# Optimization experiments

Hardware: AMD Instinct MI355X
Metric: run time of the kernel (lower is better)

The kernel has to match this reference:

```python
import jax, jax.numpy as jnp
import numpy as np

N, E, G = 50000, 800000, 64
NODE_DIM, HID, HEADS, EDGE_DIM = 128, 256, 4, 2
LAYER_IN = [NODE_DIM, HID, HID]
LAYER_HEADS = [HEADS, HEADS, 1]
BN_EPS = 1e-5


def setup_inputs() -> dict:
    key = jax.random.key(0)
    ks = iter(jax.random.split(key, 80))
    def nrm(shape, s=0.05):
        return jax.random.normal(next(ks), shape, jnp.float32) * s
    inp = {}
    inp['x'] = jax.random.normal(next(ks), (N, NODE_DIM), jnp.float32)
    inp['edge_index'] = jax.random.randint(next(ks), (2, E), 0, N, jnp.int32)
    inp['edge_attr'] = jax.random.normal(next(ks), (E, EDGE_DIM), jnp.float32)
    inp['batch'] = jnp.sort(jax.random.randint(next(ks), (N,), 0, G, jnp.int32))
    for i in range(3):
        H = LAYER_HEADS[i]; C = HID // H
        inp[f'W{i}'] = nrm((LAYER_IN[i], H * C))
        inp[f'asrc{i}'] = nrm((H, C))
        inp[f'adst{i}'] = nrm((H, C))
        inp[f'We{i}'] = nrm((EDGE_DIM, H * C))
        inp[f'aedge{i}'] = nrm((H, C))
        inp[f'bconv{i}'] = jnp.zeros((HID,), jnp.float32)
        inp[f'bn{i}_g'] = jnp.ones((HID,), jnp.float32)
        inp[f'bn{i}_b'] = jnp.zeros((HID,), jnp.float32)
        inp[f'bn{i}_m'] = nrm((HID,), 0.01)
        inp[f'bn{i}_v'] = jnp.ones((HID,), jnp.float32)
    inp['Wskip'] = nrm((NODE_DIM, HID))
    inp['bskip'] = jnp.zeros((HID,), jnp.float32)
    inp['Wp1'] = nrm((2 * HID, HID))
    inp['bp1'] = jnp.zeros((HID,), jnp.float32)
    inp['Wp2'] = nrm((HID, 1))
    inp['bp2'] = jnp.zeros((1,), jnp.float32)
    return inp


def gat_conv(x, src, dst, ea, W, a_s, a_d, We, a_e, b, H, concat):
    n = x.shape[0]
    C = W.shape[1] // H
    h = (x @ W).reshape(n, H, C)                      # [N,H,C]
    # attention logits per edge (src/dst node terms + edge term)
    al = ((h * a_s).sum(-1)[src]
          + (h * a_d).sum(-1)[dst]
          + ((ea @ We).reshape(-1, H, C) * a_e).sum(-1))  # [Et,H]
    al = jax.nn.leaky_relu(al, 0.2)
    # segment softmax over destination nodes
    amax = jax.ops.segment_max(al, dst, num_segments=n)
    ex = jnp.exp(al - amax[dst])
    den = jax.ops.segment_sum(ex, dst, num_segments=n)
    alpha = ex / (den[dst] + 1e-16)
    out = jax.ops.segment_sum(h[src] * alpha[..., None], dst, num_segments=n)  # [N,H,C]
    out = out.reshape(n, H * C) if concat else out.mean(axis=1)
    return out + b


def _forward(x, edge_index, edge_attr, batch, layer_params, Wskip, bskip, Wp1, bp1, Wp2, bp2):
    n = x.shape[0]
    # add self-loops (PyG GATConv default), edge_attr filled with mean
    loop = jnp.arange(n, dtype=edge_index.dtype)
    src = jnp.concatenate([edge_index[0], loop])
    dst = jnp.concatenate([edge_index[1], loop])
    ea = jnp.concatenate([edge_attr, jnp.broadcast_to(edge_attr.mean(0), (n, edge_attr.shape[1]))], axis=0)
    identity = x
    for i, (W, a_s, a_d, We, a_e, b, g, be, rm, rv) in enumerate(layer_params):
        layer_identity = (identity @ Wskip + bskip) if i == 0 else identity
        concat = i < 2
        H = LAYER_HEADS[i]
        h = gat_conv(x, src, dst, ea, W, a_s, a_d, We, a_e, b, H, concat)
        h = (h - rm) * jax.lax.rsqrt(rv + BN_EPS) * g + be   # BatchNorm1d (eval)
        h = jax.nn.elu(h)
        x = h + layer_identity
        identity = x
    # global mean + max pool per graph
    counts = jnp.maximum(jax.ops.segment_sum(jnp.ones((n,), x.dtype), batch, num_segments=G), 1.0)
    mean_pool = jax.ops.segment_sum(x, batch, num_segments=G) / counts[:, None]
    max_pool = jax.ops.segment_max(x, batch, num_segments=G)
    emb = jnp.concatenate([mean_pool, max_pool], axis=1)      # [G, 2*HID]
    hmid = jax.nn.relu(emb @ Wp1 + bp1)
    return hmid @ Wp2 + bp2                                   # [G, 1]


def reference(x, edge_index, edge_attr, batch,
              W0, asrc0, adst0, We0, aedge0, bconv0, bn0_g, bn0_b, bn0_m, bn0_v,
              W1, asrc1, adst1, We1, aedge1, bconv1, bn1_g, bn1_b, bn1_m, bn1_v,
              W2, asrc2, adst2, We2, aedge2, bconv2, bn2_g, bn2_b, bn2_m, bn2_v,
              Wskip, bskip, Wp1, bp1, Wp2, bp2):
    layer_params = [
        (W0, asrc0, adst0, We0, aedge0, bconv0, bn0_g, bn0_b, bn0_m, bn0_v),
        (W1, asrc1, adst1, We1, aedge1, bconv1, bn1_g, bn1_b, bn1_m, bn1_v),
        (W2, asrc2, adst2, We2, aedge2, bconv2, bn2_g, bn2_b, bn2_m, bn2_v),
    ]
    return _forward(x, edge_index, edge_attr, batch, layer_params, Wskip, bskip, Wp1, bp1, Wp2, bp2)
```

## Files before the change

### kernel.cpp

```cpp
#include <hip/hip_runtime.h>
#include <cfloat>

#define Nn 50000
#define Ee 800000
#define Etot (Ee + Nn)
#define Gg 64
#define HIDc 256
#define BN_EPS 1e-5f

typedef unsigned int   uint32;
typedef unsigned short ushort16;
typedef short  bf16x8 __attribute__((ext_vector_type(8)));
typedef float  f32x4  __attribute__((ext_vector_type(4)));

__device__ inline ushort16 f2bf(float f) {
    uint32 u = __float_as_uint(f);
    u = (u + 0x7fffu + ((u >> 16) & 1u)) >> 16;
    return (ushort16)u;
}
__device__ inline uint32 pack2(float a, float b) {
    return (uint32)f2bf(a) | ((uint32)f2bf(b) << 16);
}
__device__ inline uint32 fenc(float f) {
    uint32 b = __float_as_uint(f);
    return (b & 0x80000000u) ? ~b : (b | 0x80000000u);
}
__device__ inline float fdec(uint32 u) {
    uint32 b = (u & 0x80000000u) ? (u & 0x7fffffffu) : ~u;
    return __uint_as_float(b);
}

__device__ inline long ws_index(int c, int k, int KB) {
    int cb = c >> 4, m = c & 15, kb = k >> 5, q = (k >> 3) & 3, e = k & 7;
    return (((long)(cb * KB + kb) * 64 + q * 16 + m) << 3) + e;
}

#define CVT4 (Nn * 128 / 4)
#define CVT_BLKS ((CVT4 + 255) / 256)
#define EBKS ((Etot + 255) / 256)
__global__ __launch_bounds__(256) void prep_kernel(
        const float* __restrict__ ea, float* __restrict__ ea_s,
        const float* __restrict__ We0, const float* __restrict__ ae0,
        const float* __restrict__ We1, const float* __restrict__ ae1,
        const float* __restrict__ We2, const float* __restrict__ ae2,
        float* __restrict__ M,
        const float* __restrict__ W0, const float* __restrict__ Wskip,
        const float* __restrict__ W1, const float* __restrict__ W2,
        ushort16* __restrict__ WtC, ushort16* __restrict__ Wt1,
        ushort16* __restrict__ Wt2,
        const float* __restrict__ x, ushort16* __restrict__ xbf,
        const int* __restrict__ ei, int* __restrict__ counts) {
    int bid = blockIdx.x, t = threadIdx.x;
    if (bid < 256) {
        __shared__ float sh0[256], sh1[256];
        float s0 = 0.f, s1 = 0.f;
        for (int e = bid * 256 + t; e < Ee; e += 256 * 256) {
            s0 += ea[2 * e];
            s1 += ea[2 * e + 1];
        }
        sh0[t] = s0; sh1[t] = s1;
        __syncthreads();
        for (int off = 128; off > 0; off >>= 1) {
            if (t < off) { sh0[t] += sh0[t + off]; sh1[t] += sh1[t + off]; }
            __syncthreads();
        }
        if (t == 0) { atomicAdd(&ea_s[0], sh0[0]); atomicAdd(&ea_s[1], sh1[0]); }
    } else if (bid == 256) {
        if (t >= 18) return;
        int l = t < 8 ? 0 : (t < 16 ? 1 : 2);
        int r = t - l * 8;
        const float* We = (l == 0) ? We0 : (l == 1 ? We1 : We2);
        const float* ae = (l == 0) ? ae0 : (l == 1 ? ae1 : ae2);
        int Hl = (l < 2) ? 4 : 1;
        int Cl = 256 / Hl;
        int d = r / Hl, hh = r % Hl;
        float s = 0.f;
        for (int c = 0; c < Cl; ++c)
            s += We[d * 256 + hh * Cl + c] * ae[hh * Cl + c];
        M[l * 8 + r] = s;
    } else if (bid < 385) {
        int k = bid - 257;
        WtC[ws_index(t, k, 4)] = f2bf(W0[(long)k * 256 + t]);
    } else if (bid < 513) {
        int k = bid - 385;
        WtC[ws_index(256 + t, k, 4)] = f2bf(Wskip[(long)k * 256 + t]);
    } else if (bid < 769) {
        int k = bid - 513;
        Wt1[ws_index(t, k, 8)] = f2bf(W1[(long)k * 256 + t]);
    } else if (bid < 1025) {
        int k = bid - 769;
        Wt2[ws_index(t, k, 8)] = f2bf(W2[(long)k * 256 + t]);
    } else if (bid < 1025 + CVT_BLKS) {
        int i = (bid - 1025) * 256 + t;
        if (i < CVT4) {
            float4 v = *(const float4*)&x[i * 4];
            ushort4 o;
            o.x = f2bf(v.x); o.y = f2bf(v.y); o.z = f2bf(v.z); o.w = f2bf(v.w);
            *(ushort4*)&xbf[i * 4] = o;
        }
    } else {
        int e = (bid - 1025 - CVT_BLKS) * 256 + t;
        if (e < Etot) {
            int d = (e < Ee) ? ei[Ee + e] : (e - Ee);
            atomicAdd(&counts[d], 1);
        }
    }
}

__global__ void scan1_kernel(const int* __restrict__ in, int* __restrict__ inc,
                             int* __restrict__ bsums) {
    __shared__ int sh[256];
    int i = blockIdx.x * 256 + threadIdx.x;
    int v = (i < Nn) ? in[i] : 0;
    sh[threadIdx.x] = v;
    __syncthreads();
    for (int off = 1; off < 256; off <<= 1) {
        int t = ((int)threadIdx.x >= off) ? sh[threadIdx.x - off] : 0;
        __syncthreads();
        sh[threadIdx.x] += t;
        __syncthreads();
    }
    if (i < Nn) inc[i] = sh[threadIdx.x];
    if (threadIdx.x == 255) bsums[blockIdx.x] = sh[255];
}

__global__ void scan23_kernel(const int* __restrict__ inc, const int* __restrict__ bsums,
                              int* __restrict__ row_start, int* __restrict__ cursor, int nb) {
    __shared__ int sh[256];
    int b = blockIdx.x, t = threadIdx.x;
    sh[t] = (t < b && t < nb) ? bsums[t] : 0;
    __syncthreads();
    for (int off = 128; off > 0; off >>= 1) {
        if (t < off) sh[t] += sh[t + off];
        __syncthreads();
    }
    int base = sh[0];
    int i = b * 256 + t;
    if (i < Nn) {
        int v = inc[i] + base;
        row_start[i + 1] = v;
        cursor[i + 1] = v;
    }
    if (i == 0) { row_start[0] = 0; cursor[0] = 0; }
}

__global__ void scatter_kernel(const int* __restrict__ ei, const float* __restrict__ ea,
                               const float* __restrict__ ea_sum, int* __restrict__ cursor,
                               int* __restrict__ src_sorted, float* __restrict__ ea_sorted) {
    int e = blockIdx.x * blockDim.x + threadIdx.x;
    if (e >= Etot) return;
    int s, d; float e0, e1;
    if (e < Ee) {
        s = ei[e]; d = ei[Ee + e];
        e0 = ea[2 * e]; e1 = ea[2 * e + 1];
    } else {
        s = d = e - Ee;
        const float invE = 1.f / (float)Ee;
        e0 = ea_sum[0] * invE; e1 = ea_sum[1] * invE;
    }
    int pos = atomicAdd(&cursor[d], 1);
    src_sorted[pos] = s;
    ea_sorted[2 * pos]     = e0;
    ea_sorted[2 * pos + 1] = e1;
}

#define LDK 40
__global__ __launch_bounds__(256) void mfma_gemm_kernel(
        const ushort16* __restrict__ A,
        const ushort16* __restrict__ WS,
        uint32* __restrict__ outF,
        uint32* __restrict__ outS,
        const float* __restrict__ bskip,
        const float* __restrict__ a_s, const float* __restrict__ a_d,
        float* __restrict__ ssrc, float* __restrict__ sdst,
        int n, int K) {
    __shared__ ushort16 As[128 * LDK];
    const int t    = threadIdx.x;
    const int row0 = blockIdx.x * 128;
    const int c0   = blockIdx.y * 128;
    const bool isSkip = (outS != nullptr) && (c0 >= 256);
    const int cc0  = isSkip ? c0 - 256 : c0;
    const int wave = t >> 6, lane = t & 63;
    const int wr = wave >> 1, wc = wave & 1;
    const int l15 = lane & 15, quad = lane >> 4;
    const int KB = K >> 5;

    f32x4 acc[4][4];
#pragma unroll
    for (int j = 0; j < 4; ++j)
#pragma unroll
        for (int i = 0; i < 4; ++i) {
            acc[j][i][0] = 0.f; acc[j][i][1] = 0.f;
            acc[j][i][2] = 0.f; acc[j][i][3] = 0.f;
        }

    const int sm = t & 127;
    const int so = t >> 7;

    for (int k0 = 0; k0 < K; k0 += 32) {
        const int kb = k0 >> 5;
#pragma unroll
        for (int h = 0; h < 2; ++h) {
            int oct = so + 2 * h;
            int grow = row0 + sm;
            uint4 va = make_uint4(0, 0, 0, 0);
            if (grow < n) va = *(const uint4*)&A[(long)grow * K + k0 + 8 * oct];
            *(uint4*)&As[sm * LDK + 8 * oct] = va;
        }
        bf16x8 bfv[4];
#pragma unroll
        for (int j = 0; j < 4; ++j) {
            int cb = ((c0 + wc * 64) >> 4) + j;
            bfv[j] = *(const bf16x8*)&WS[(((long)cb * KB + kb) * 64 + lane) << 3];
        }
        __syncthreads();
        bf16x8 af[4];
#pragma unroll
        for (int i = 0; i < 4; ++i)
            af[i] = *(const bf16x8*)&As[(wr * 64 + i * 16 + l15) * LDK + quad * 8];
#pragma unroll
        for (int j = 0; j < 4; ++j)
#pragma unroll
            for (int i = 0; i < 4; ++i)
                acc[j][i] = __builtin_amdgcn_mfma_f32_16x16x32_bf16(
                    bfv[j], af[i], acc[j][i], 0, 0, 0);
        __syncthreads();
    }

    float4 bb[4];
#pragma unroll
    for (int j = 0; j < 4; ++j) {
        if (isSkip) bb[j] = *(const float4*)&bskip[cc0 + wc * 64 + j * 16 + quad * 4];
        else        bb[j] = make_float4(0.f, 0.f, 0.f, 0.f);
    }

    uint32* tgt = isSkip ? outS : outF;
#pragma unroll
    for (int i = 0; i < 4; ++i) {
        int row = row0 + wr * 64 + i * 16 + l15;
        if (row >= n) continue;
#pragma unroll
        for (int j = 0; j < 4; ++j) {
            int col = cc0 + wc * 64 + j * 16 + quad * 4;
            uint2 pk;
            pk.x = pack2(acc[j][i][0] + bb[j].x, acc[j][i][1] + bb[j].y);
            pk.y = pack2(acc[j][i][2] + bb[j].z, acc[j][i][3] + bb[j].w);
            *(uint2*)&tgt[(long)row * 128 + (col >> 1)] = pk;
        }
    }

    if (!isSkip && a_s != nullptr) {
        float4 asv[4], adv[4];
#pragma unroll
        for (int j = 0; j < 4; ++j) {
            int col = cc0 + wc * 64 + j * 16 + quad * 4;
            asv[j] = *(const float4*)&a_s[col];
            adv[j] = *(const float4*)&a_d[col];
        }
        const int part = (cc0 + wc * 64) >> 6;
#pragma unroll
        for (int i = 0; i < 4; ++i) {
            float ps = 0.f, pd = 0.f;
#pragma unroll
            for (int j = 0; j < 4; ++j) {
                ps += acc[j][i][0] * asv[j].x + acc[j][i][1] * asv[j].y
                    + acc[j][i][2] * asv[j].z + acc[j][i][3] * asv[j].w;
                pd += acc[j][i][0] * adv[j].x + acc[j][i][1] * adv[j].y
                    + acc[j][i][2] * adv[j].z + acc[j][i][3] * adv[j].w;
            }
            ps += __shfl_xor(ps, 16); ps += __shfl_xor(ps, 32);
            pd += __shfl_xor(pd, 16); pd += __shfl_xor(pd, 32);
            if (quad == 0) {
                int row = row0 + wr * 64 + i * 16 + l15;
                if (row < n) {
                    ssrc[row * 4 + part] = ps;
                    sdst[row * 4 + part] = pd;
                }
            }
        }
    }
}

template <int H>
__global__ __launch_bounds__(128) void agg_kernel(
        const int* __restrict__ src_sorted, const int* __restrict__ row_start,
        const float* __restrict__ ea_sorted, const float* __restrict__ ssrc,
        const float* __restrict__ sdst, const float* __restrict__ M,
        float* __restrict__ wbig,
        const uint32* __restrict__ hbuf2, const float* __restrict__ bconv,
        const float* __restrict__ bn_g, const float* __restrict__ bn_b,
        const float* __restrict__ bn_m, const float* __restrict__ bn_v,
        const uint32* __restrict__ identity2, uint32* __restrict__ out2) {
    __shared__ float shw[256 * H];
    int node = blockIdx.x;
    int t = threadIdx.x;
    int beg = row_start[node], end = row_start[node + 1];
    int deg = end - beg;
    bool big = deg > 256;

    if (t < 64) {
        int lane = t;
        float sd[H], M0[H], M1[H], m[H], den[H];
        if (H == 4) {
#pragma unroll
            for (int h = 0; h < H; ++h) sd[h] = sdst[node * 4 + h];
        } else {
            float4 v = *(const float4*)&sdst[node * 4];
            sd[0] = v.x + v.y + v.z + v.w;
        }
#pragma unroll
        for (int h = 0; h < H; ++h) {
            M0[h] = M[h]; M1[h] = M[H + h];
            m[h] = -FLT_MAX; den[h] = 0.f;
        }
        auto ssval = [&](int s, int h) -> float {
            if (H == 4) return ssrc[s * 4 + h];
            float4 v = *(const float4*)&ssrc[s * 4];
            return v.x + v.y + v.z + v.w;
        };
        if (!big) {
            float lreg[4][H];
#pragma unroll
            for (int k = 0; k < 4; ++k) {
                int idx = beg + lane + (k << 6);
                if (idx < end) {
                    int s = src_sorted[idx];
                    float e0 = ea_sorted[2 * idx], e1 = ea_sorted[2 * idx + 1];
#pragma unroll
                    for (int h = 0; h < H; ++h) {
                        float l = ssval(s, h) + sd[h] + e0 * M0[h] + e1 * M1[h];
                        l = (l > 0.f) ? l : 0.2f * l;
                        lreg[k][h] = l;
                        if (l > m[h]) { den[h] = den[h] * __expf(m[h] - l) + 1.f; m[h] = l; }
                        else den[h] += __expf(l - m[h]);
                    }
                }
            }
#pragma unroll
            for (int h = 0; h < H; ++h) {
                for (int off = 32; off > 0; off >>= 1) {
                    float om = __shfl_down(m[h], off);
                    float od = __shfl_down(den[h], off);
                    float nm = fmaxf(m[h], om);
                    den[h] = den[h] * __expf(m[h] - nm) + od * __expf(om - nm);
                    m[h] = nm;
                }
                m[h]   = __shfl(m[h], 0);
                den[h] = __shfl(den[h], 0);
                den[h] = 1.f / (den[h] + 1e-16f);
            }
#pragma unroll
            for (int k = 0; k < 4; ++k) {
                int idx = beg + lane + (k << 6);
                if (idx < end) {
#pragma unroll
                    for (int h = 0; h < H; ++h)
                        shw[(idx - beg) * H + h] = __expf(lreg[k][h] - m[h]) * den[h];
                }
            }
        } else {
            for (int idx = beg + lane; idx < end; idx += 64) {
                int s = src_sorted[idx];
                float e0 = ea_sorted[2 * idx], e1 = ea_sorted[2 * idx + 1];
#pragma unroll
                for (int h = 0; h < H; ++h) {
                    float l = ssval(s, h) + sd[h] + e0 * M0[h] + e1 * M1[h];
                    l = (l > 0.f) ? l : 0.2f * l;
                    wbig[(long)idx * H + h] = l;
                    if (l > m[h]) { den[h] = den[h] * __expf(m[h] - l) + 1.f; m[h] = l; }
                    else den[h] += __expf(l - m[h]);
                }
            }
#pragma unroll
            for (int h = 0; h < H; ++h) {
                for (int off = 32; off > 0; off >>= 1) {
                    float om = __shfl_down(m[h], off);
                    float od = __shfl_down(den[h], off);
                    float nm = fmaxf(m[h], om);
                    den[h] = den[h] * __expf(m[h] - nm) + od * __expf(om - nm);
                    m[h] = nm;
                }
                m[h]   = __shfl(m[h], 0);
                den[h] = __shfl(den[h], 0);
                den[h] = 1.f / (den[h] + 1e-16f);
            }
            for (int idx = beg + lane; idx < end; idx += 64) {
#pragma unroll
                for (int h = 0; h < H; ++h) {
                    float l = wbig[(long)idx * H + h];
                    wbig[(long)idx * H + h] = __expf(l - m[h]) * den[h];
                }
            }
        }
    }
    __syncthreads();

    int c2 = t;
    const int C2 = 128 / H;
    int hh = c2 / C2;
    float a0 = 0.f, a1 = 0.f;
    for (int idx = beg; idx < end; idx += 4) {
        int   s[4];
        float ww[4];
#pragma unroll
        for (int k = 0; k < 4; ++k) {
            int j = idx + k;
            bool ok = j < end;
            int jj = ok ? j : beg;
            s[k]  = src_sorted[jj];
            float wv = big ? wbig[(long)jj * H + hh] : shw[(jj - beg) * H + hh];
            ww[k] = ok ? wv : 0.f;
        }
#pragma unroll
        for (int k = 0; k < 4; ++k) {
            uint32 u = hbuf2[(long)s[k] * 128 + c2];
            float lo = __uint_as_float(u << 16);
            float hi = __uint_as_float(u & 0xffff0000u);
            a0 += ww[k] * lo;
            a1 += ww[k] * hi;
        }
    }
    int c = 2 * c2;
    float v0 = a0 + bconv[c];
    float v1 = a1 + bconv[c + 1];
    v0 = (v0 - bn_m[c])     * rsqrtf(bn_v[c]     + BN_EPS) * bn_g[c]     + bn_b[c];
    v1 = (v1 - bn_m[c + 1]) * rsqrtf(bn_v[c + 1] + BN_EPS) * bn_g[c + 1] + bn_b[c + 1];
    v0 = (v0 > 0.f) ? v0 : (expf(v0) - 1.f);
    v1 = (v1 > 0.f) ? v1 : (expf(v1) - 1.f);
    uint32 idu = identity2[(long)node * 128 + c2];
    v0 += __uint_as_float(idu << 16);
    v1 += __uint_as_float(idu & 0xffff0000u);
    out2[(long)node * 128 + c2] = pack2(v0, v1);
}

#define POOL_ROWS 32
__global__ __launch_bounds__(128) void pool_kernel(
        const uint32* __restrict__ x2, const int* __restrict__ batch,
        float* __restrict__ psum, uint32* __restrict__ pmax, float* __restrict__ pcnt) {
    int c2 = threadIdx.x;
    int n0 = blockIdx.x * POOL_ROWS;
    if (n0 >= Nn) return;
    int n1 = min(n0 + POOL_ROWS, Nn);
    int cur = batch[n0];
    float s0 = 0.f, s1 = 0.f, m0 = -FLT_MAX, m1 = -FLT_MAX;
    int cnt = 0;
    int c = 2 * c2;
    for (int i = n0; i < n1; ++i) {
        int g = batch[i];
        if (g != cur) {
            atomicAdd(&psum[cur * 256 + c], s0);
            atomicAdd(&psum[cur * 256 + c + 1], s1);
            atomicMax(&pmax[cur * 256 + c], fenc(m0));
            atomicMax(&pmax[cur * 256 + c + 1], fenc(m1));
            if (c2 == 0) atomicAdd(&pcnt[cur], (float)cnt);
            cur = g; s0 = s1 = 0.f; m0 = m1 = -FLT_MAX; cnt = 0;
        }
        uint32 u = x2[(long)i * 128 + c2];
        float lo = __uint_as_float(u << 16);
        float hi = __uint_as_float(u & 0xffff0000u);
        s0 += lo; s1 += hi;
        m0 = fmaxf(m0, lo); m1 = fmaxf(m1, hi);
        ++cnt;
    }
    atomicAdd(&psum[cur * 256 + c], s0);
    atomicAdd(&psum[cur * 256 + c + 1], s1);
    atomicMax(&pmax[cur * 256 + c], fenc(m0));
    atomicMax(&pmax[cur * 256 + c + 1], fenc(m1));
    if (c2 == 0) atomicAdd(&pcnt[cur], (float)cnt);
}

__global__ __launch_bounds__(256) void mlp_kernel(
        const float* __restrict__ psum, const uint32* __restrict__ pmax,
        const float* __restrict__ pcnt, const float* __restrict__ Wp1,
        const float* __restrict__ bp1, const float* __restrict__ Wp2,
        const float* __restrict__ bp2, float* __restrict__ out) {
    int g = blockIdx.x;
    int j = threadIdx.x;
    float inv = 1.f / fmaxf(pcnt[g], 1.f);
    float acc = bp1[j];
    for (int k = 0; k < 256; ++k)
        acc += (psum[g * 256 + k] * inv) * Wp1[k * 256 + j];
    for (int k = 0; k < 256; ++k)
        acc += fdec(pmax[g * 256 + k]) * Wp1[(256 + k) * 256 + j];
    float v = fmaxf(acc, 0.f) * Wp2[j];
    __shared__ float red[256];
    red[j] = v;
    __syncthreads();
    for (int off = 128; off > 0; off >>= 1) {
        if (j < off) red[j] += red[j + off];
        __syncthreads();
    }
    if (j == 0) out[g] = red[0] + bp2[0];
}

extern "C" void kernel_launch(void* const* d_in, const int* in_sizes, int n_in,
                              void* d_out, int out_size, void* d_ws, size_t ws_size,
                              hipStream_t stream) {
    const float* x   = (const float*)d_in[0];
    const int*   ei  = (const int*)d_in[1];
    const float* ea  = (const float*)d_in[2];
    const int*   bat = (const int*)d_in[3];
    auto LP = [&](int l, int j) { return (const float*)d_in[4 + l * 10 + j]; };
    const float* Wskip = (const float*)d_in[34];
    const float* bskip = (const float*)d_in[35];
    const float* Wp1   = (const float*)d_in[36];
    const float* bp1   = (const float*)d_in[37];
    const float* Wp2   = (const float*)d_in[38];
    const float* bp2   = (const float*)d_in[39];
    float* out = (float*)d_out;

    char* p = (char*)d_ws;
    auto alloc = [&](size_t bytes) { void* r = (void*)p; p += (bytes + 255) & ~(size_t)255; return r; };
    uint32*   hbuf2  = (uint32*)alloc((size_t)Nn * 256 * 2);
    uint32*   skipbf = (uint32*)alloc((size_t)Nn * 128 * 4);
    uint32*   resA   = (uint32*)alloc((size_t)Nn * 128 * 4);
    uint32*   resB   = (uint32*)alloc((size_t)Nn * 128 * 4);
    ushort16* xbf    = (ushort16*)alloc((size_t)Nn * 128 * 2);
    float*    wbuf   = (float*)alloc((size_t)Etot * 4 * 4);
    float*    ea_sorted = (float*)alloc((size_t)Etot * 2 * 4);
    float*    ssrc   = (float*)alloc((size_t)Nn * 4 * 4);
    float*    sdst   = (float*)alloc((size_t)Nn * 4 * 4);
    int*      counts = (int*)alloc((size_t)Nn * 4);
    int*      incb   = (int*)alloc((size_t)Nn * 4);
    int*      row_start = (int*)alloc((size_t)(Nn + 1) * 4);
    int*      cursor    = (int*)alloc((size_t)(Nn + 1) * 4);
    int*      src_sorted = (int*)alloc((size_t)Etot * 4);
    int*      bsums  = (int*)alloc(256 * 4);
    float*    ea_s   = (float*)alloc(2 * 4);
    float*    Mbuf   = (float*)alloc(32 * 4);
    ushort16* WtC    = (ushort16*)alloc((size_t)512 * 128 * 2);
    ushort16* Wt1    = (ushort16*)alloc((size_t)256 * 256 * 2);
    ushort16* Wt2    = (ushort16*)alloc((size_t)256 * 256 * 2);
    float*    psum   = (float*)alloc((size_t)Gg * 256 * 4);
    uint32*   pmax   = (uint32*)alloc((size_t)Gg * 256 * 4);
    float*    pcnt   = (float*)alloc((size_t)Gg * 4);

    const int nb = (Nn + 255) / 256;

    hipMemsetAsync(counts, 0, (size_t)Nn * 4, stream);
    hipMemsetAsync(ea_s, 0, 8, stream);
    hipMemsetAsync(psum, 0, (size_t)Gg * 256 * 4 * 2 + (size_t)Gg * 4, stream);

    prep_kernel<<<1025 + CVT_BLKS + EBKS, 256, 0, stream>>>(
        ea, ea_s, LP(0,3), LP(0,4), LP(1,3), LP(1,4), LP(2,3), LP(2,4), Mbuf,
        LP(0,0), Wskip, LP(1,0), LP(2,0), WtC, Wt1, Wt2, x, xbf, ei, counts);

    scan1_kernel<<<nb, 256, 0, stream>>>(counts, incb, bsums);
    scan23_kernel<<<nb, 256, 0, stream>>>(incb, bsums, row_start, cursor, nb);
    scatter_kernel<<<EBKS, 256, 0, stream>>>(ei, ea, ea_s, cursor, src_sorted, ea_sorted);

    {
        dim3 g0((Nn + 127) / 128, 4);
        mfma_gemm_kernel<<<g0, 256, 0, stream>>>(
            xbf, WtC, hbuf2, skipbf, bskip,
            LP(0,1), LP(0,2), ssrc, sdst, Nn, 128);
    }

    const uint32* lid[3] = { skipbf, resA, resB };
    uint32*       lou[3] = { resA, resB, resA };
    const int     Hh[3]  = { 4, 4, 1 };
    const ushort16* lain[3] = { nullptr, (ushort16*)resA, (ushort16*)resB };
    const ushort16* lwt[3]  = { nullptr, Wt1, Wt2 };
    for (int l = 0; l < 3; ++l) {
        const int H = Hh[l];
        if (l > 0) {
            dim3 gl((Nn + 127) / 128, 2);
            mfma_gemm_kernel<<<gl, 256, 0, stream>>>(
                lain[l], lwt[l], hbuf2, nullptr, nullptr,
                LP(l,1), LP(l,2), ssrc, sdst, Nn, 256);
        }
        if (H == 4)
            agg_kernel<4><<<Nn, 128, 0, stream>>>(
                src_sorted, row_start, ea_sorted, ssrc, sdst, Mbuf + l * 8, wbuf,
                hbuf2, LP(l,5), LP(l,6), LP(l,7), LP(l,8), LP(l,9), lid[l], lou[l]);
        else
            agg_kernel<1><<<Nn, 128, 0, stream>>>(
                src_sorted, row_start, ea_sorted, ssrc, sdst, Mbuf + l * 8, wbuf,
                hbuf2, LP(l,5), LP(l,6), LP(l,7), LP(l,8), LP(l,9), lid[l], lou[l]);
    }

    pool_kernel<<<(Nn + POOL_ROWS - 1) / POOL_ROWS, 128, 0, stream>>>(resA, bat, psum, pmax, pcnt);
    mlp_kernel<<<Gg, 256, 0, stream>>>(psum, pmax, pcnt, Wp1, bp1, Wp2, bp2, out);
}
```

Before: 709.0 us.

## Split GAT edge softmax into separate wave-per-node kernel before aggregation

Moves the per-destination edge softmax out of the aggregation kernel into its own kernel, where each 64-lane wave handles one node and four nodes share a 256-thread block. The normalized weights go to a global buffer, and the aggregation kernel reads them from there instead of from shared memory. Before, half the threads in each 128-thread block sat idle during the softmax phase and a block-wide barrier was needed. The cost is one extra launch per layer plus a global write and reread of all edge weights.

```diff
diff --git a/kernel.cpp b/kernel.cpp
--- a/kernel.cpp
+++ b/kernel.cpp
@@ -282,122 +282,122 @@
 }
 
 template <int H>
-__global__ __launch_bounds__(128) void agg_kernel(
+__global__ __launch_bounds__(256) void edge_softmax_kernel(
         const int* __restrict__ src_sorted, const int* __restrict__ row_start,
         const float* __restrict__ ea_sorted, const float* __restrict__ ssrc,
         const float* __restrict__ sdst, const float* __restrict__ M,
-        float* __restrict__ wbig,
-        const uint32* __restrict__ hbuf2, const float* __restrict__ bconv,
-        const float* __restrict__ bn_g, const float* __restrict__ bn_b,
-        const float* __restrict__ bn_m, const float* __restrict__ bn_v,
-        const uint32* __restrict__ identity2, uint32* __restrict__ out2) {
-    __shared__ float shw[256 * H];
-    int node = blockIdx.x;
-    int t = threadIdx.x;
+        float* __restrict__ w) {
+    int node = (blockIdx.x * blockDim.x + threadIdx.x) >> 6;
+    int lane = threadIdx.x & 63;
+    if (node >= Nn) return;
     int beg = row_start[node], end = row_start[node + 1];
     int deg = end - beg;
-    bool big = deg > 256;
-
-    if (t < 64) {
-        int lane = t;
-        float sd[H], M0[H], M1[H], m[H], den[H];
-        if (H == 4) {
-#pragma unroll
-            for (int h = 0; h < H; ++h) sd[h] = sdst[node * 4 + h];
-        } else {
-            float4 v = *(const float4*)&sdst[node * 4];
-            sd[0] = v.x + v.y + v.z + v.w;
-        }
-#pragma unroll
-        for (int h = 0; h < H; ++h) {
-            M0[h] = M[h]; M1[h] = M[H + h];
-            m[h] = -FLT_MAX; den[h] = 0.f;
-        }
-        auto ssval = [&](int s, int h) -> float {
-            if (H == 4) return ssrc[s * 4 + h];
-            float4 v = *(const float4*)&ssrc[s * 4];
-            return v.x + v.y + v.z + v.w;
-        };
-        if (!big) {
-            float lreg[4][H];
-#pragma unroll
-            for (int k = 0; k < 4; ++k) {
-                int idx = beg + lane + (k << 6);
-                if (idx < end) {
-                    int s = src_sorted[idx];
-                    float e0 = ea_sorted[2 * idx], e1 = ea_sorted[2 * idx + 1];
-#pragma unroll
-                    for (int h = 0; h < H; ++h) {
-                        float l = ssval(s, h) + sd[h] + e0 * M0[h] + e1 * M1[h];
-                        l = (l > 0.f) ? l : 0.2f * l;
-                        lreg[k][h] = l;
-                        if (l > m[h]) { den[h] = den[h] * __expf(m[h] - l) + 1.f; m[h] = l; }
-                        else den[h] += __expf(l - m[h]);
-                    }
-                }
-            }
-#pragma unroll
-            for (int h = 0; h < H; ++h) {
-                for (int off = 32; off > 0; off >>= 1) {
-                    float om = __shfl_down(m[h], off);
-                    float od = __shfl_down(den[h], off);
-                    float nm = fmaxf(m[h], om);
-                    den[h] = den[h] * __expf(m[h] - nm) + od * __expf(om - nm);
-                    m[h] = nm;
-                }
-                m[h]   = __shfl(m[h], 0);
-                den[h] = __shfl(den[h], 0);
-                den[h] = 1.f / (den[h] + 1e-16f);
-            }
-#pragma unroll
-            for (int k = 0; k < 4; ++k) {
-                int idx = beg + lane + (k << 6);
-                if (idx < end) {
-#pragma unroll
-                    for (int h = 0; h < H; ++h)
-                        shw[(idx - beg) * H + h] = __expf(lreg[k][h] - m[h]) * den[h];
-                }
-            }
-        } else {
-            for (int idx = beg + lane; idx < end; idx += 64) {
+    float sd[H], M0[H], M1[H], m[H], den[H];
+    if (H == 4) {
+#pragma unroll
+        for (int h = 0; h < H; ++h) sd[h] = sdst[node * 4 + h];
+    } else {
+        float4 v = *(const float4*)&sdst[node * 4];
+        sd[0] = v.x + v.y + v.z + v.w;
+    }
+#pragma unroll
+    for (int h = 0; h < H; ++h) {
+        M0[h] = M[h]; M1[h] = M[H + h];
+        m[h] = -FLT_MAX; den[h] = 0.f;
+    }
+    auto ssval = [&](int s, int h) -> float {
+        if (H == 4) return ssrc[s * 4 + h];
+        float4 v = *(const float4*)&ssrc[s * 4];
+        return v.x + v.y + v.z + v.w;
+    };
+    if (deg <= 256) {
+        float lreg[4][H];
+#pragma unroll
+        for (int k = 0; k < 4; ++k) {
+            int idx = beg + lane + (k << 6);
+            if (idx < end) {
                 int s = src_sorted[idx];
                 float e0 = ea_sorted[2 * idx], e1 = ea_sorted[2 * idx + 1];
 #pragma unroll
                 for (int h = 0; h < H; ++h) {
                     float l = ssval(s, h) + sd[h] + e0 * M0[h] + e1 * M1[h];
                     l = (l > 0.f) ? l : 0.2f * l;
-                    wbig[(long)idx * H + h] = l;
+                    lreg[k][h] = l;
                     if (l > m[h]) { den[h] = den[h] * __expf(m[h] - l) + 1.f; m[h] = l; }
                     else den[h] += __expf(l - m[h]);
                 }
             }
+        }
+#pragma unroll
+        for (int h = 0; h < H; ++h) {
+            for (int off = 32; off > 0; off >>= 1) {
+                float om = __shfl_down(m[h], off);
+                float od = __shfl_down(den[h], off);
+                float nm = fmaxf(m[h], om);
+                den[h] = den[h] * __expf(m[h] - nm) + od * __expf(om - nm);
+                m[h] = nm;
+            }
+            m[h]   = __shfl(m[h], 0);
+            den[h] = __shfl(den[h], 0);
+            den[h] = 1.f / (den[h] + 1e-16f);
+        }
+#pragma unroll
+        for (int k = 0; k < 4; ++k) {
+            int idx = beg + lane + (k << 6);
+            if (idx < end) {
+#pragma unroll
+                for (int h = 0; h < H; ++h)
+                    w[(long)idx * H + h] = __expf(lreg[k][h] - m[h]) * den[h];
+            }
+        }
+    } else {
+        for (int idx = beg + lane; idx < end; idx += 64) {
+            int s = src_sorted[idx];
+            float e0 = ea_sorted[2 * idx], e1 = ea_sorted[2 * idx + 1];
 #pragma unroll
             for (int h = 0; h < H; ++h) {
-                for (int off = 32; off > 0; off >>= 1) {
-                    float om = __shfl_down(m[h], off);
-                    float od = __shfl_down(den[h], off);
-                    float nm = fmaxf(m[h], om);
-                    den[h] = den[h] * __expf(m[h] - nm) + od * __expf(om - nm);
-                    m[h] = nm;
-                }
-                m[h]   = __shfl(m[h], 0);
-                den[h] = __shfl(den[h], 0);
-                den[h] = 1.f / (den[h] + 1e-16f);
-            }
-            for (int idx = beg + lane; idx < end; idx += 64) {
-#pragma unroll
-                for (int h = 0; h < H; ++h) {
-                    float l = wbig[(long)idx * H + h];
-                    wbig[(long)idx * H + h] = __expf(l - m[h]) * den[h];
-                }
-            }
-        }
-    }
-    __syncthreads();
-
-    int c2 = t;
-    const int C2 = 128 / H;
+                float l = ssval(s, h) + sd[h] + e0 * M0[h] + e1 * M1[h];
+                l = (l > 0.f) ? l : 0.2f * l;
+                w[(long)idx * H + h] = l;
+                if (l > m[h]) { den[h] = den[h] * __expf(m[h] - l) + 1.f; m[h] = l; }
+                else den[h] += __expf(l - m[h]);
+            }
+        }
+#pragma unroll
+        for (int h = 0; h < H; ++h) {
+            for (int off = 32; off > 0; off >>= 1) {
+                float om = __shfl_down(m[h], off);
+                float od = __shfl_down(den[h], off);
+                float nm = fmaxf(m[h], om);
+                den[h] = den[h] * __expf(m[h] - nm) + od * __expf(om - nm);
+                m[h] = nm;
+            }
+            m[h]   = __shfl(m[h], 0);
+            den[h] = __shfl(den[h], 0);
+            den[h] = 1.f / (den[h] + 1e-16f);
+        }
+        for (int idx = beg + lane; idx < end; idx += 64) {
+#pragma unroll
+            for (int h = 0; h < H; ++h) {
+                float l = w[(long)idx * H + h];
+                w[(long)idx * H + h] = __expf(l - m[h]) * den[h];
+            }
+        }
+    }
+}
+
+__global__ __launch_bounds__(128) void agg_kernel(
+        const int* __restrict__ src_sorted, const int* __restrict__ row_start,
+        const uint32* __restrict__ hbuf2, const float* __restrict__ w,
+        const float* __restrict__ bconv,
+        const float* __restrict__ bn_g, const float* __restrict__ bn_b,
+        const float* __restrict__ bn_m, const float* __restrict__ bn_v,
+        const uint32* __restrict__ identity2, uint32* __restrict__ out2, int H) {
+    int node = blockIdx.x;
+    int c2 = threadIdx.x;
+    int C2 = 128 / H;
     int hh = c2 / C2;
+    int beg = row_start[node], end = row_start[node + 1];
     float a0 = 0.f, a1 = 0.f;
     for (int idx = beg; idx < end; idx += 4) {
         int   s[4];
@@ -408,8 +408,7 @@
             bool ok = j < end;
             int jj = ok ? j : beg;
             s[k]  = src_sorted[jj];
-            float wv = big ? wbig[(long)jj * H + hh] : shw[(jj - beg) * H + hh];
-            ww[k] = ok ? wv : 0.f;
+            ww[k] = ok ? w[(long)jj * H + hh] : 0.f;
         }
 #pragma unroll
         for (int k = 0; k < 4; ++k) {
@@ -536,6 +535,7 @@
     float*    pcnt   = (float*)alloc((size_t)Gg * 4);
 
     const int nb = (Nn + 255) / 256;
+    const int wgrid = (Nn * 64 + 255) / 256;
 
     hipMemsetAsync(counts, 0, (size_t)Nn * 4, stream);
     hipMemsetAsync(ea_s, 0, 8, stream);
@@ -570,13 +570,13 @@
                 LP(l,1), LP(l,2), ssrc, sdst, Nn, 256);
         }
         if (H == 4)
-            agg_kernel<4><<<Nn, 128, 0, stream>>>(
-                src_sorted, row_start, ea_sorted, ssrc, sdst, Mbuf + l * 8, wbuf,
-                hbuf2, LP(l,5), LP(l,6), LP(l,7), LP(l,8), LP(l,9), lid[l], lou[l]);
+            edge_softmax_kernel<4><<<wgrid, 256, 0, stream>>>(
+                src_sorted, row_start, ea_sorted, ssrc, sdst, Mbuf + l * 8, wbuf);
         else
-            agg_kernel<1><<<Nn, 128, 0, stream>>>(
-                src_sorted, row_start, ea_sorted, ssrc, sdst, Mbuf + l * 8, wbuf,
-                hbuf2, LP(l,5), LP(l,6), LP(l,7), LP(l,8), LP(l,9), lid[l], lou[l]);
+            edge_softmax_kernel<1><<<wgrid, 256, 0, stream>>>(
+                src_sorted, row_start, ea_sorted, ssrc, sdst, Mbuf + l * 8, wbuf);
+        agg_kernel<<<Nn, 128, 0, stream>>>(src_sorted, row_start, hbuf2, wbuf,
+            LP(l,5), LP(l,6), LP(l,7), LP(l,8), LP(l,9), lid[l], lou[l], H);
     }
 
     pool_kernel<<<(Nn + POOL_ROWS - 1) / POOL_ROWS, 128, 0, stream>>>(resA, bat, psum, pmax, pcnt);
```

Result: no change. 705.0 us (-0.6%).
